# Kernel tuning notes

Hardware: AMD Instinct MI355X
Metric: run time of the kernel (lower is better)

The kernel has to match this reference:

```python
import jax, jax.numpy as jnp
import numpy as np

B, S, H, E = 32, 4096, 512, 512

def setup_inputs() -> dict:
    key = jax.random.key(0)
    ks = jax.random.split(key, 11)
    sc = 1.0 / np.sqrt(H)
    return {
        "context": jax.random.normal(ks[0], (B, S, H), jnp.float32),
        "h": jax.random.normal(ks[1], (B, H), jnp.float32),
        "x": jax.random.normal(ks[2], (B, E), jnp.float32),
        "We": jax.random.normal(ks[3], (H, H), jnp.float32) * sc,
        "be": jax.random.normal(ks[4], (H,), jnp.float32) * sc,
        "Wd": jax.random.normal(ks[5], (H, H), jnp.float32) * sc,
        "bd": jax.random.normal(ks[6], (H,), jnp.float32) * sc,
        "Wv": jax.random.normal(ks[7], (H,), jnp.float32) * sc,
        "bv": jax.random.normal(ks[8], (1,), jnp.float32) * sc,
        "Wr": jax.random.normal(ks[9], (2 * H, 2 * H + E), jnp.float32) * (1.0 / np.sqrt(2 * H + E)),
        "br": jax.random.normal(ks[10], (2 * H,), jnp.float32) * sc,
    }

def reference(context, h, x, We, be, Wd, bd, Wv, bv, Wr, br):
    # gamma_encoder: [B,S,H]; gamma_decoder: [B,1,H]
    ge = jnp.einsum('bsh,kh->bsk', context, We) + be
    gd = h @ Wd.T + bd
    # additive scores -> [B,S]
    scores = jnp.einsum('bsh,h->bs', jnp.tanh(ge + gd[:, None, :]), Wv) + bv[0]
    weights = jax.nn.softmax(scores, axis=1)
    # context vector c_t: [B,H]
    c_t = jnp.einsum('bs,bsh->bh', weights, context)
    # linear_r on [c_t, h, x] -> [B,2H]
    r_t = jnp.concatenate([c_t, h, x], axis=1) @ Wr.T + br
    # maxout over pairs: view [B,H,2].max(-1)
    output = jnp.max(r_t.reshape(-1, r_t.shape[1] // 2, 2), axis=2)
    return (output, weights)
```

## Files before the change

kernel.cpp:

```cpp
#include <hip/hip_runtime.h>

typedef __attribute__((ext_vector_type(8))) short bf16x8;
typedef __attribute__((ext_vector_type(16))) float f32x16;

typedef __attribute__((address_space(3))) unsigned int lds_u32;
typedef __attribute__((address_space(1))) unsigned int glb_u32;

union frag_u { bf16x8 v; unsigned int u[4]; };

__device__ inline unsigned int cvt_pk_bf16(float lo, float hi){
  unsigned int r;
  asm("v_cvt_pk_bf16_f32 %0, %1, %2" : "=v"(r) : "v"(lo), "v"(hi));
  return r;
}
__device__ inline bf16x8 pack8(float4 a, float4 b){
  union { unsigned int u[4]; bf16x8 v; } r;
  r.u[0]=cvt_pk_bf16(a.x,a.y); r.u[1]=cvt_pk_bf16(a.z,a.w);
  r.u[2]=cvt_pk_bf16(b.x,b.y); r.u[3]=cvt_pk_bf16(b.z,b.w);
  return r.v;
}
__device__ inline float fast_tanh(float x){
  float e = __builtin_amdgcn_exp2f(x * 2.8853900817779268f);
  return 1.0f - 2.0f * __builtin_amdgcn_rcpf(e + 1.0f);
}
#define PIN8(F) asm volatile("" : "+v"((F).u[0]), "+v"((F).u[1]), \
                                  "+v"((F).u[2]), "+v"((F).u[3]))
#define LOG2E 1.4426950408889634f

__global__ __launch_bounds__(256) void we_conv(const float* __restrict__ We,
                                               uint4* __restrict__ weFrag){
  int gid = blockIdx.x * 256 + threadIdx.x;
  int l  = gid & 63;
  int nc = gid >> 11;
  int t  = (gid >> 6) & 31;
  int colv = nc*32 + (l & 31);
  int k = t*16 + (l >> 5)*8;
  const float4* src = (const float4*)(We + colv*512 + k);
  float4 f0 = src[0], f1 = src[1];
  weFrag[gid] = make_uint4(cvt_pk_bf16(f0.x,f0.y), cvt_pk_bf16(f0.z,f0.w),
                           cvt_pk_bf16(f1.x,f1.y), cvt_pk_bf16(f1.z,f1.w));
}

__global__ __launch_bounds__(256) void gd_kernel(const float* __restrict__ hvec,
                                                 const float* __restrict__ Wd,
                                                 const float* __restrict__ bd,
                                                 const float* __restrict__ be,
                                                 float* __restrict__ gd){
  __shared__ float hs[512];
  int b = blockIdx.x >> 2, kc = blockIdx.x & 3;
  int tid = threadIdx.x;
  hs[tid]       = hvec[b*512 + tid];
  hs[tid + 256] = hvec[b*512 + 256 + tid];
  __syncthreads();
  int k  = kc*128 + (tid >> 1);
  int hh = (tid & 1) * 256;
  const float4* wrow = (const float4*)(Wd + (size_t)k*512 + hh);
  const float4* hv4  = (const float4*)(hs + hh);
  float acc = 0.f;
  #pragma unroll 8
  for (int i = 0; i < 64; ++i){
    float4 w = wrow[i]; float4 u = hv4[i];
    acc += w.x*u.x + w.y*u.y + w.z*u.z + w.w*u.w;
  }
  acc += __shfl_xor(acc, 1);
  if ((tid & 1) == 0) gd[b*512 + k] = acc + bd[k] + be[k];
}

__global__ __launch_bounds__(256, 2) void score_kernel(
    const float* __restrict__ ctx, const uint4* __restrict__ weFrag,
    const float* __restrict__ gd, const float* __restrict__ Wv,
    float* __restrict__ scores, float* __restrict__ ctp,
    float* __restrict__ MS){
  __shared__ char lds[2*32768 + 4096];
  __shared__ float sc_lds[128];
  __shared__ float w_lds[128];
  __shared__ float red2[2];
  char* ldsB = lds;
  float* gdwv = (float*)(lds + 65536);

  const int tid  = threadIdx.x;
  const int wid  = tid >> 6;
  const int lane = tid & 63;
  const int bid  = blockIdx.x;
  const int row0 = bid * 128;
  const int b    = bid >> 5;
  const int col  = lane & 31;
  const int hi   = lane >> 5;
  const int st   = bid & 15;

  #define ISSUE(NC, BUF) do { \
    const char* _g = (const char*)weFrag + (size_t)(NC)*32768 + wid*8192 + lane*16; \
    char* _l = ldsB + (BUF)*32768 + wid*8192; \
    _Pragma("unroll") \
    for (int _i = 0; _i < 8; ++_i) \
      __builtin_amdgcn_global_load_lds((const glb_u32*)(_g + _i*1024), \
                                       (lds_u32*)(_l + _i*1024), 16, 0, 0); \
  } while(0)

  ISSUE(st, 0);

  if (tid < 128) ((float4*)gdwv)[tid] = ((const float4*)(gd + b*512))[tid];
  else           ((float4*)gdwv)[tid] = ((const float4*)Wv)[tid - 128];

  frag_u afrag[32];
  {
    const float4* ap = (const float4*)(ctx + (size_t)(row0 + wid*32 + col)*512 + hi*8);
    #pragma unroll
    for (int t = 0; t < 32; ++t){
      afrag[t].v = pack8(ap[t*4], ap[t*4 + 1]);
      PIN8(afrag[t]);
    }
  }

  asm volatile("s_waitcnt lgkmcnt(0)" ::: "memory");

  float sc[16];
  #pragma unroll
  for (int r = 0; r < 16; ++r) sc[r] = 0.f;

  for (int nc = 0; nc < 16; ++nc){
    const int cur = (st + nc) & 15;
    asm volatile("s_waitcnt vmcnt(0)" ::: "memory");
    __builtin_amdgcn_s_barrier();
    if (nc < 15) ISSUE((cur + 1) & 15, (nc + 1) & 1);

    const char* bb = ldsB + (nc & 1)*32768 + lane*16;
    f32x16 a0v, a1v, a2v, a3v;
    #pragma unroll
    for (int r = 0; r < 16; ++r){ a0v[r]=0.f; a1v[r]=0.f; a2v[r]=0.f; a3v[r]=0.f; }

    __builtin_amdgcn_s_setprio(1);
    #pragma unroll
    for (int t = 0; t < 8; ++t){
      bf16x8 b0 = *(const bf16x8*)(bb + (t     )*1024);
      bf16x8 b1 = *(const bf16x8*)(bb + (t +  8)*1024);
      bf16x8 b2 = *(const bf16x8*)(bb + (t + 16)*1024);
      bf16x8 b3 = *(const bf16x8*)(bb + (t + 24)*1024);
      a0v = __builtin_amdgcn_mfma_f32_32x32x16_bf16(afrag[t     ].v, b0, a0v, 0, 0, 0);
      a1v = __builtin_amdgcn_mfma_f32_32x32x16_bf16(afrag[t +  8].v, b1, a1v, 0, 0, 0);
      a2v = __builtin_amdgcn_mfma_f32_32x32x16_bf16(afrag[t + 16].v, b2, a2v, 0, 0, 0);
      a3v = __builtin_amdgcn_mfma_f32_32x32x16_bf16(afrag[t + 24].v, b3, a3v, 0, 0, 0);
    }
    __builtin_amdgcn_s_setprio(0);

    float gdv = gdwv[cur*32 + col];
    float wvv = gdwv[512 + cur*32 + col];
    #pragma unroll
    for (int r = 0; r < 16; ++r)
      sc[r] += fast_tanh(((a0v[r] + a1v[r]) + (a2v[r] + a3v[r])) + gdv) * wvv;
  }
  #undef ISSUE

  #pragma unroll
  for (int r = 0; r < 16; ++r){
    #pragma unroll
    for (int m = 1; m <= 16; m <<= 1) sc[r] += __shfl_xor(sc[r], m);
  }
  if (col == 0){
    float* so = scores + row0 + wid*32 + 4*hi;
    #pragma unroll
    for (int r = 0; r < 16; ++r){
      int rr = (r & 3) + 8*(r >> 2);
      so[rr] = sc[r];
      sc_lds[wid*32 + 4*hi + rr] = sc[r];
    }
  }
  __syncthreads();

  float M = -1e30f;
  {
    const float4* s4 = (const float4*)sc_lds;
    #pragma unroll
    for (int i = 0; i < 32; ++i){
      float4 v = s4[i];
      M = fmaxf(M, fmaxf(fmaxf(v.x, v.y), fmaxf(v.z, v.w)));
    }
  }
  if (tid < 128){
    float w = __builtin_amdgcn_exp2f((sc_lds[tid] - M) * LOG2E);
    w_lds[tid] = w;
    #pragma unroll
    for (int o = 1; o < 64; o <<= 1) w += __shfl_xor(w, o);
    if ((tid & 63) == 0) red2[tid >> 6] = w;
  }
  __syncthreads();
  float S_blk = red2[0] + red2[1];

  float ctpA = 0.f, ctpB = 0.f;
  #pragma unroll
  for (int p = 0; p < 2; ++p){
    if ((wid >> 1) == p){
      int rl = (wid & 1)*32 + col;
      char* dst = ldsB + rl*1024;
      int swz = (rl & 7) << 4;
      #pragma unroll
      for (int t = 0; t < 32; ++t)
        *(uint4*)(dst + ((t*32 + hi*16) ^ swz)) = *(uint4*)&afrag[t].u[0];
    }
    __syncthreads();
    const float* wp = w_lds + p*64;
    #pragma unroll 8
    for (int r = 0; r < 64; ++r){
      unsigned int u = *(const unsigned int*)(ldsB + r*1024 + ((tid*4) ^ ((r & 7) << 4)));
      float cw = wp[r];
      union { unsigned int q; float f; } flo, fhi;
      flo.q = u << 16;
      fhi.q = u & 0xffff0000u;
      ctpA += cw * flo.f;
      ctpB += cw * fhi.f;
    }
    __syncthreads();
  }
  ((float2*)(ctp + (size_t)bid*512))[tid] = make_float2(ctpA, ctpB);
  if (tid == 0){ MS[2*bid] = M; MS[2*bid + 1] = S_blk; }
}

__global__ __launch_bounds__(256) void combine_kernel(const float* __restrict__ ctp,
                                                      const float* __restrict__ MS,
                                                      float* __restrict__ ct,
                                                      float* __restrict__ mbuf){
  __shared__ float wsh[32];
  __shared__ float msh[2];
  int b = blockIdx.x, tid = threadIdx.x;
  if (tid < 64){
    int i = tid & 31;
    float Mi = MS[(b*32 + i)*2];
    float Si = MS[(b*32 + i)*2 + 1];
    float M = Mi;
    #pragma unroll
    for (int o = 1; o < 32; o <<= 1) M = fmaxf(M, __shfl_xor(M, o));
    float w = __builtin_amdgcn_exp2f((Mi - M) * LOG2E);
    float d = w * Si;
    #pragma unroll
    for (int o = 1; o < 32; o <<= 1) d += __shfl_xor(d, o);
    if (tid < 32) wsh[i] = w;
    if (tid == 0){ msh[0] = M; msh[1] = 1.0f / d; }
  }
  __syncthreads();
  float invd = msh[1];
  float a0 = 0.f, a1 = 0.f;
  #pragma unroll
  for (int i = 0; i < 32; ++i){
    float2 v = ((const float2*)(ctp + (size_t)(b*32 + i)*512))[tid];
    float w = wsh[i];
    a0 += w * v.x; a1 += w * v.y;
  }
  ((float2*)(ct + b*512))[tid] = make_float2(a0 * invd, a1 * invd);
  if (tid == 0){ mbuf[2*b] = msh[0]; mbuf[2*b + 1] = invd; }
}

__global__ __launch_bounds__(256) void weights_kernel(const float* __restrict__ scores,
                                                      const float* __restrict__ mbuf,
                                                      float* __restrict__ weights){
  int b = blockIdx.x, tid = threadIdx.x;
  float M = mbuf[2*b], invd = mbuf[2*b + 1];
  const float4* src = (const float4*)(scores + b*4096);
  float4* dst = (float4*)(weights + b*4096);
  #pragma unroll
  for (int i = 0; i < 4; ++i){
    float4 v = src[tid + i*256];
    v.x = __builtin_amdgcn_exp2f((v.x - M) * LOG2E) * invd;
    v.y = __builtin_amdgcn_exp2f((v.y - M) * LOG2E) * invd;
    v.z = __builtin_amdgcn_exp2f((v.z - M) * LOG2E) * invd;
    v.w = __builtin_amdgcn_exp2f((v.w - M) * LOG2E) * invd;
    dst[tid + i*256] = v;
  }
}

__global__ __launch_bounds__(256) void final_kernel(
    const float* __restrict__ ct, const float* __restrict__ hvec,
    const float* __restrict__ x, const float* __restrict__ Wr,
    const float* __restrict__ br, float* __restrict__ out){
  __shared__ float xs[8][1536];
  int bt = blockIdx.x >> 4;
  int it = blockIdx.x & 15;
  int tid = threadIdx.x;
  int b0 = bt * 8;
  for (int idx = tid; idx < 8*1536; idx += 256){
    int bl = idx / 1536, j = idx % 1536;
    int b = b0 + bl;
    float v = (j < 512) ? ct[b*512 + j]
            : (j < 1024) ? hvec[b*512 + (j - 512)]
            : x[b*512 + (j - 1024)];
    xs[bl][j] = v;
  }
  __syncthreads();
  int i = it*64 + (tid & 63);
  int bl0 = (tid >> 6) * 2;
  const float4* wrow = (const float4*)(Wr + (size_t)i*1536);
  const float4* x0 = (const float4*)xs[bl0];
  const float4* x1 = (const float4*)xs[bl0 + 1];
  float a0 = 0.f, a1 = 0.f;
  #pragma unroll 4
  for (int k = 0; k < 384; ++k){
    float4 w = wrow[k];
    float4 u0 = x0[k], u1 = x1[k];
    a0 += w.x*u0.x + w.y*u0.y + w.z*u0.z + w.w*u0.w;
    a1 += w.x*u1.x + w.y*u1.y + w.z*u1.z + w.w*u1.w;
  }
  float bias = br[i];
  a0 += bias; a1 += bias;
  float n0 = __shfl_xor(a0, 1);
  float n1 = __shfl_xor(a1, 1);
  if ((tid & 1) == 0){
    out[(b0 + bl0    )*512 + (i >> 1)] = fmaxf(a0, n0);
    out[(b0 + bl0 + 1)*512 + (i >> 1)] = fmaxf(a1, n1);
  }
}

extern "C" void kernel_launch(void* const* d_in, const int* in_sizes, int n_in,
                              void* d_out, int out_size, void* d_ws, size_t ws_size,
                              hipStream_t stream){
  const float* ctx  = (const float*)d_in[0];
  const float* hvec = (const float*)d_in[1];
  const float* x    = (const float*)d_in[2];
  const float* We   = (const float*)d_in[3];
  const float* be   = (const float*)d_in[4];
  const float* Wd   = (const float*)d_in[5];
  const float* bd   = (const float*)d_in[6];
  const float* Wv   = (const float*)d_in[7];
  const float* Wr   = (const float*)d_in[9];
  const float* br   = (const float*)d_in[10];

  float* out     = (float*)d_out;
  float* weights = out + 32*512;

  char* ws = (char*)d_ws;
  char* weFrag   = ws;
  float* scores  = (float*)(ws + (512 << 10));
  float* ctp     = (float*)(ws + (1024 << 10));
  float* MS      = (float*)(ws + (3 << 20));
  float* mbuf    = (float*)(ws + (3 << 20) + (16 << 10));
  float* ct      = (float*)(ws + (3 << 20) + (32 << 10));
  float* gd      = (float*)(ws + (3 << 20) + (96 << 10));

  we_conv<<<128, 256, 0, stream>>>(We, (uint4*)weFrag);
  gd_kernel<<<128, 256, 0, stream>>>(hvec, Wd, bd, be, gd);
  score_kernel<<<1024, 256, 0, stream>>>(ctx, (const uint4*)weFrag, gd, Wv,
                                         scores, ctp, MS);
  combine_kernel<<<32, 256, 0, stream>>>(ctp, MS, ct, mbuf);
  weights_kernel<<<32, 256, 0, stream>>>(scores, mbuf, weights);
  final_kernel<<<64, 256, 0, stream>>>(ct, hvec, x, Wr, br, out);
}
```

Before: 204.2 us.

## Triple-buffer half-chunk We loads and overlap tanh epilogue with next chunk MFMAs

Splits each 32KB We chunk into two 16KB halves held in a three-slot LDS ring, with two halves kept in flight ahead of use. The tanh/score epilogue of the previous chunk is deferred and interleaved between the MFMA groups of the next chunk, so transcendental work can overlap matrix work. LDS drops from about 68KB to about 52KB, which could allow more resident blocks. The context-vector staging now runs in four passes of 32 rows to fit the smaller buffer, which adds barriers.

```diff
diff --git a/kernel.cpp b/kernel.cpp
--- a/kernel.cpp
+++ b/kernel.cpp
@@ -71,12 +71,11 @@
     const float* __restrict__ gd, const float* __restrict__ Wv,
     float* __restrict__ scores, float* __restrict__ ctp,
     float* __restrict__ MS){
-  __shared__ char lds[2*32768 + 4096];
+  __shared__ char ldsB[3*16384];
+  __shared__ float gdwv[1024];
   __shared__ float sc_lds[128];
   __shared__ float w_lds[128];
   __shared__ float red2[2];
-  char* ldsB = lds;
-  float* gdwv = (float*)(lds + 65536);
 
   const int tid  = threadIdx.x;
   const int wid  = tid >> 6;
@@ -88,16 +87,18 @@
   const int hi   = lane >> 5;
   const int st   = bid & 15;
 
-  #define ISSUE(NC, BUF) do { \
-    const char* _g = (const char*)weFrag + (size_t)(NC)*32768 + wid*8192 + lane*16; \
-    char* _l = ldsB + (BUF)*32768 + wid*8192; \
+  #define ISSUE_L(HCL) do { \
+    int _gh = (((st + ((HCL) >> 1)) & 15) << 1) | ((HCL) & 1); \
+    const char* _g = (const char*)weFrag + (size_t)_gh*16384 + wid*4096 + lane*16; \
+    char* _l = ldsB + ((HCL) % 3)*16384 + wid*4096; \
     _Pragma("unroll") \
-    for (int _i = 0; _i < 8; ++_i) \
+    for (int _i = 0; _i < 4; ++_i) \
       __builtin_amdgcn_global_load_lds((const glb_u32*)(_g + _i*1024), \
                                        (lds_u32*)(_l + _i*1024), 16, 0, 0); \
   } while(0)
 
-  ISSUE(st, 0);
+  ISSUE_L(0);
+  ISSUE_L(1);
 
   if (tid < 128) ((float4*)gdwv)[tid] = ((const float4*)(gd + b*512))[tid];
   else           ((float4*)gdwv)[tid] = ((const float4*)Wv)[tid - 128];
@@ -114,42 +115,76 @@
 
   asm volatile("s_waitcnt lgkmcnt(0)" ::: "memory");
 
-  float sc[16];
+  float sc[16], pend[16];
+  float pGd = 0.f, pWv = 0.f;
   #pragma unroll
   for (int r = 0; r < 16; ++r) sc[r] = 0.f;
+
+  f32x16 a0v, a1v, a2v, a3v;
+
+  #define MGROUP(BB, H, TG) do { \
+    const char* _bb = (BB); \
+    bf16x8 b0 = *(const bf16x8*)(_bb + ((TG)*4 + 0)*1024); \
+    bf16x8 b1 = *(const bf16x8*)(_bb + ((TG)*4 + 1)*1024); \
+    bf16x8 b2 = *(const bf16x8*)(_bb + ((TG)*4 + 2)*1024); \
+    bf16x8 b3 = *(const bf16x8*)(_bb + ((TG)*4 + 3)*1024); \
+    a0v = __builtin_amdgcn_mfma_f32_32x32x16_bf16(afrag[(H)*16 + (TG)*4 + 0].v, b0, a0v, 0, 0, 0); \
+    a1v = __builtin_amdgcn_mfma_f32_32x32x16_bf16(afrag[(H)*16 + (TG)*4 + 1].v, b1, a1v, 0, 0, 0); \
+    a2v = __builtin_amdgcn_mfma_f32_32x32x16_bf16(afrag[(H)*16 + (TG)*4 + 2].v, b2, a2v, 0, 0, 0); \
+    a3v = __builtin_amdgcn_mfma_f32_32x32x16_bf16(afrag[(H)*16 + (TG)*4 + 3].v, b3, a3v, 0, 0, 0); \
+  } while(0)
+
+  #define TANH4(TG) do { \
+    sc[(TG)*4 + 0] += fast_tanh(pend[(TG)*4 + 0] + pGd) * pWv; \
+    sc[(TG)*4 + 1] += fast_tanh(pend[(TG)*4 + 1] + pGd) * pWv; \
+    sc[(TG)*4 + 2] += fast_tanh(pend[(TG)*4 + 2] + pGd) * pWv; \
+    sc[(TG)*4 + 3] += fast_tanh(pend[(TG)*4 + 3] + pGd) * pWv; \
+  } while(0)
 
   for (int nc = 0; nc < 16; ++nc){
     const int cur = (st + nc) & 15;
-    asm volatile("s_waitcnt vmcnt(0)" ::: "memory");
+    const int hc  = 2*nc;
+
+    #pragma unroll
+    for (int r = 0; r < 16; ++r){ a0v[r]=0.f; a1v[r]=0.f; a2v[r]=0.f; a3v[r]=0.f; }
+
+    asm volatile("s_waitcnt vmcnt(4)" ::: "memory");
     __builtin_amdgcn_s_barrier();
-    if (nc < 15) ISSUE((cur + 1) & 15, (nc + 1) & 1);
-
-    const char* bb = ldsB + (nc & 1)*32768 + lane*16;
-    f32x16 a0v, a1v, a2v, a3v;
-    #pragma unroll
-    for (int r = 0; r < 16; ++r){ a0v[r]=0.f; a1v[r]=0.f; a2v[r]=0.f; a3v[r]=0.f; }
-
-    __builtin_amdgcn_s_setprio(1);
-    #pragma unroll
-    for (int t = 0; t < 8; ++t){
-      bf16x8 b0 = *(const bf16x8*)(bb + (t     )*1024);
-      bf16x8 b1 = *(const bf16x8*)(bb + (t +  8)*1024);
-      bf16x8 b2 = *(const bf16x8*)(bb + (t + 16)*1024);
-      bf16x8 b3 = *(const bf16x8*)(bb + (t + 24)*1024);
-      a0v = __builtin_amdgcn_mfma_f32_32x32x16_bf16(afrag[t     ].v, b0, a0v, 0, 0, 0);
-      a1v = __builtin_amdgcn_mfma_f32_32x32x16_bf16(afrag[t +  8].v, b1, a1v, 0, 0, 0);
-      a2v = __builtin_amdgcn_mfma_f32_32x32x16_bf16(afrag[t + 16].v, b2, a2v, 0, 0, 0);
-      a3v = __builtin_amdgcn_mfma_f32_32x32x16_bf16(afrag[t + 24].v, b3, a3v, 0, 0, 0);
-    }
-    __builtin_amdgcn_s_setprio(0);
-
-    float gdv = gdwv[cur*32 + col];
-    float wvv = gdwv[512 + cur*32 + col];
+    if (nc < 15) ISSUE_L(hc + 2);
+    {
+      const char* bb = ldsB + (hc % 3)*16384 + lane*16;
+      __builtin_amdgcn_s_setprio(1);
+      MGROUP(bb, 0, 0); if (nc > 0) TANH4(0);
+      MGROUP(bb, 0, 1); if (nc > 0) TANH4(1);
+      MGROUP(bb, 0, 2); if (nc > 0) TANH4(2);
+      MGROUP(bb, 0, 3); if (nc > 0) TANH4(3);
+      __builtin_amdgcn_s_setprio(0);
+    }
+
+    if (nc < 15) asm volatile("s_waitcnt vmcnt(4)" ::: "memory");
+    else         asm volatile("s_waitcnt vmcnt(0)" ::: "memory");
+    __builtin_amdgcn_s_barrier();
+    if (nc < 15) ISSUE_L(hc + 3);
+    {
+      const char* bb = ldsB + ((hc + 1) % 3)*16384 + lane*16;
+      __builtin_amdgcn_s_setprio(1);
+      MGROUP(bb, 1, 0);
+      MGROUP(bb, 1, 1);
+      MGROUP(bb, 1, 2);
+      MGROUP(bb, 1, 3);
+      __builtin_amdgcn_s_setprio(0);
+    }
+
     #pragma unroll
     for (int r = 0; r < 16; ++r)
-      sc[r] += fast_tanh(((a0v[r] + a1v[r]) + (a2v[r] + a3v[r])) + gdv) * wvv;
-  }
-  #undef ISSUE
+      pend[r] = (a0v[r] + a1v[r]) + (a2v[r] + a3v[r]);
+    pGd = gdwv[cur*32 + col];
+    pWv = gdwv[512 + cur*32 + col];
+  }
+  TANH4(0); TANH4(1); TANH4(2); TANH4(3);
+  #undef ISSUE_L
+  #undef MGROUP
+  #undef TANH4
 
   #pragma unroll
   for (int r = 0; r < 16; ++r){
@@ -188,9 +223,9 @@
 
   float ctpA = 0.f, ctpB = 0.f;
   #pragma unroll
-  for (int p = 0; p < 2; ++p){
-    if ((wid >> 1) == p){
-      int rl = (wid & 1)*32 + col;
+  for (int p = 0; p < 4; ++p){
+    if (wid == p){
+      int rl = col;
       char* dst = ldsB + rl*1024;
       int swz = (rl & 7) << 4;
       #pragma unroll
@@ -198,9 +233,9 @@
         *(uint4*)(dst + ((t*32 + hi*16) ^ swz)) = *(uint4*)&afrag[t].u[0];
     }
     __syncthreads();
-    const float* wp = w_lds + p*64;
+    const float* wp = w_lds + p*32;
     #pragma unroll 8
-    for (int r = 0; r < 64; ++r){
+    for (int r = 0; r < 32; ++r){
       unsigned int u = *(const unsigned int*)(ldsB + r*1024 + ((tid*4) ^ ((r & 7) << 4)));
       float cw = wp[r];
       union { unsigned int q; float f; } flo, fhi;
```

After: 206.1 us. No clear change (+0.9%).

## Double score block to 512 threads sharing each We chunk across 256 rows

Applied to the files above, without the earlier changes.

The score kernel now runs 512-thread blocks covering 256 context rows each, so every We chunk staged in LDS is shared by eight waves instead of four. Each wave issues half as many global-to-LDS loads, which halves total We traffic into LDS. Launch bounds change to (512,1), the MFMA priority hints are removed, and the context-partial pass gives each thread one column. The combine kernel is reworked for 16 partials per batch. The trade-off is a larger block with more barrier participants and possibly different occupancy, given the large per-thread A-fragment register footprint.

```diff
diff --git a/kernel.cpp b/kernel.cpp
--- a/kernel.cpp
+++ b/kernel.cpp
@@ -66,41 +66,40 @@
   if ((tid & 1) == 0) gd[b*512 + k] = acc + bd[k] + be[k];
 }
 
-__global__ __launch_bounds__(256, 2) void score_kernel(
+__global__ __launch_bounds__(512, 1) void score_kernel(
     const float* __restrict__ ctx, const uint4* __restrict__ weFrag,
     const float* __restrict__ gd, const float* __restrict__ Wv,
     float* __restrict__ scores, float* __restrict__ ctp,
     float* __restrict__ MS){
-  __shared__ char lds[2*32768 + 4096];
-  __shared__ float sc_lds[128];
-  __shared__ float w_lds[128];
-  __shared__ float red2[2];
-  char* ldsB = lds;
-  float* gdwv = (float*)(lds + 65536);
+  __shared__ char ldsB[2*32768];
+  __shared__ float gdwv[1024];
+  __shared__ float sc_lds[256];
+  __shared__ float w_lds[256];
+  __shared__ float red4[4];
 
   const int tid  = threadIdx.x;
   const int wid  = tid >> 6;
   const int lane = tid & 63;
   const int bid  = blockIdx.x;
-  const int row0 = bid * 128;
-  const int b    = bid >> 5;
+  const int row0 = bid * 256;
+  const int b    = bid >> 4;
   const int col  = lane & 31;
   const int hi   = lane >> 5;
   const int st   = bid & 15;
 
   #define ISSUE(NC, BUF) do { \
-    const char* _g = (const char*)weFrag + (size_t)(NC)*32768 + wid*8192 + lane*16; \
-    char* _l = ldsB + (BUF)*32768 + wid*8192; \
+    const char* _g = (const char*)weFrag + (size_t)(NC)*32768 + wid*4096 + lane*16; \
+    char* _l = ldsB + (BUF)*32768 + wid*4096; \
     _Pragma("unroll") \
-    for (int _i = 0; _i < 8; ++_i) \
+    for (int _i = 0; _i < 4; ++_i) \
       __builtin_amdgcn_global_load_lds((const glb_u32*)(_g + _i*1024), \
                                        (lds_u32*)(_l + _i*1024), 16, 0, 0); \
   } while(0)
 
   ISSUE(st, 0);
 
-  if (tid < 128) ((float4*)gdwv)[tid] = ((const float4*)(gd + b*512))[tid];
-  else           ((float4*)gdwv)[tid] = ((const float4*)Wv)[tid - 128];
+  if (tid < 128)      ((float4*)gdwv)[tid] = ((const float4*)(gd + b*512))[tid];
+  else if (tid < 256) ((float4*)gdwv)[tid] = ((const float4*)Wv)[tid - 128];
 
   frag_u afrag[32];
   {
@@ -129,7 +128,6 @@
     #pragma unroll
     for (int r = 0; r < 16; ++r){ a0v[r]=0.f; a1v[r]=0.f; a2v[r]=0.f; a3v[r]=0.f; }
 
-    __builtin_amdgcn_s_setprio(1);
     #pragma unroll
     for (int t = 0; t < 8; ++t){
       bf16x8 b0 = *(const bf16x8*)(bb + (t     )*1024);
@@ -141,7 +139,6 @@
       a2v = __builtin_amdgcn_mfma_f32_32x32x16_bf16(afrag[t + 16].v, b2, a2v, 0, 0, 0);
       a3v = __builtin_amdgcn_mfma_f32_32x32x16_bf16(afrag[t + 24].v, b3, a3v, 0, 0, 0);
     }
-    __builtin_amdgcn_s_setprio(0);
 
     float gdv = gdwv[cur*32 + col];
     float wvv = gdwv[512 + cur*32 + col];
@@ -171,24 +168,24 @@
   {
     const float4* s4 = (const float4*)sc_lds;
     #pragma unroll
-    for (int i = 0; i < 32; ++i){
+    for (int i = 0; i < 64; ++i){
       float4 v = s4[i];
       M = fmaxf(M, fmaxf(fmaxf(v.x, v.y), fmaxf(v.z, v.w)));
     }
   }
-  if (tid < 128){
+  if (tid < 256){
     float w = __builtin_amdgcn_exp2f((sc_lds[tid] - M) * LOG2E);
     w_lds[tid] = w;
     #pragma unroll
     for (int o = 1; o < 64; o <<= 1) w += __shfl_xor(w, o);
-    if ((tid & 63) == 0) red2[tid >> 6] = w;
-  }
-  __syncthreads();
-  float S_blk = red2[0] + red2[1];
-
-  float ctpA = 0.f, ctpB = 0.f;
-  #pragma unroll
-  for (int p = 0; p < 2; ++p){
+    if ((tid & 63) == 0) red4[tid >> 6] = w;
+  }
+  __syncthreads();
+  float S_blk = red4[0] + red4[1] + red4[2] + red4[3];
+
+  float ctp1 = 0.f;
+  #pragma unroll
+  for (int p = 0; p < 4; ++p){
     if ((wid >> 1) == p){
       int rl = (wid & 1)*32 + col;
       char* dst = ldsB + rl*1024;
@@ -201,17 +198,13 @@
     const float* wp = w_lds + p*64;
     #pragma unroll 8
     for (int r = 0; r < 64; ++r){
-      unsigned int u = *(const unsigned int*)(ldsB + r*1024 + ((tid*4) ^ ((r & 7) << 4)));
-      float cw = wp[r];
-      union { unsigned int q; float f; } flo, fhi;
-      flo.q = u << 16;
-      fhi.q = u & 0xffff0000u;
-      ctpA += cw * flo.f;
-      ctpB += cw * fhi.f;
+      unsigned int u = *(const unsigned short*)(ldsB + r*1024 + ((tid*2) ^ ((r & 7) << 4)));
+      union { unsigned int q; float f; } fv; fv.q = u << 16;
+      ctp1 += wp[r] * fv.f;
     }
     __syncthreads();
   }
-  ((float2*)(ctp + (size_t)bid*512))[tid] = make_float2(ctpA, ctpB);
+  ctp[(size_t)bid*512 + tid] = ctp1;
   if (tid == 0){ MS[2*bid] = M; MS[2*bid + 1] = S_blk; }
 }
 
@@ -219,29 +212,28 @@
                                                       const float* __restrict__ MS,
                                                       float* __restrict__ ct,
                                                       float* __restrict__ mbuf){
-  __shared__ float wsh[32];
+  __shared__ float wsh[16];
   __shared__ float msh[2];
   int b = blockIdx.x, tid = threadIdx.x;
-  if (tid < 64){
-    int i = tid & 31;
-    float Mi = MS[(b*32 + i)*2];
-    float Si = MS[(b*32 + i)*2 + 1];
+  if (tid < 16){
+    float Mi = MS[(b*16 + tid)*2];
+    float Si = MS[(b*16 + tid)*2 + 1];
     float M = Mi;
     #pragma unroll
-    for (int o = 1; o < 32; o <<= 1) M = fmaxf(M, __shfl_xor(M, o));
+    for (int o = 1; o < 16; o <<= 1) M = fmaxf(M, __shfl_xor(M, o));
     float w = __builtin_amdgcn_exp2f((Mi - M) * LOG2E);
     float d = w * Si;
     #pragma unroll
-    for (int o = 1; o < 32; o <<= 1) d += __shfl_xor(d, o);
-    if (tid < 32) wsh[i] = w;
+    for (int o = 1; o < 16; o <<= 1) d += __shfl_xor(d, o);
+    wsh[tid] = w;
     if (tid == 0){ msh[0] = M; msh[1] = 1.0f / d; }
   }
   __syncthreads();
   float invd = msh[1];
   float a0 = 0.f, a1 = 0.f;
   #pragma unroll
-  for (int i = 0; i < 32; ++i){
-    float2 v = ((const float2*)(ctp + (size_t)(b*32 + i)*512))[tid];
+  for (int i = 0; i < 16; ++i){
+    float2 v = ((const float2*)(ctp + (size_t)(b*16 + i)*512))[tid];
     float w = wsh[i];
     a0 += w * v.x; a1 += w * v.y;
   }
@@ -336,8 +328,8 @@
 
   we_conv<<<128, 256, 0, stream>>>(We, (uint4*)weFrag);
   gd_kernel<<<128, 256, 0, stream>>>(hvec, Wd, bd, be, gd);
-  score_kernel<<<1024, 256, 0, stream>>>(ctx, (const uint4*)weFrag, gd, Wv,
-                                         scores, ctp, MS);
+  score_kernel<<<512, 512, 0, stream>>>(ctx, (const uint4*)weFrag, gd, Wv,
+                                        scores, ctp, MS);
   combine_kernel<<<32, 256, 0, stream>>>(ctp, MS, ct, mbuf);
   weights_kernel<<<32, 256, 0, stream>>>(scores, mbuf, weights);
   final_kernel<<<64, 256, 0, stream>>>(ct, hvec, x, Wr, br, out);
```

Result: no change. 206.6 us (+1.2%).

## Triple-buffer half-chunk We loads and store context partials as bf16

Applied to the files above, without the earlier changes.

The We fragment layout is reordered into 16 KB half-chunks, and the score loop uses a three-stage LDS ring with partial vmcnt waits, so the next loads stay in flight while the MFMAs run. One accumulator is used instead of four, and the per-block start-offset rotation is dropped. The context-vector partials are written as packed bf16, which halves the partial traffic into the combine kernel and adds extra rounding. LDS use drops, which may help occupancy, but there are twice as many barriers and the MFMA dependency chain is serialized.

```diff
diff --git a/kernel.cpp b/kernel.cpp
--- a/kernel.cpp
+++ b/kernel.cpp
@@ -5,8 +5,6 @@
 
 typedef __attribute__((address_space(3))) unsigned int lds_u32;
 typedef __attribute__((address_space(1))) unsigned int glb_u32;
-
-union frag_u { bf16x8 v; unsigned int u[4]; };
 
 __device__ inline unsigned int cvt_pk_bf16(float lo, float hi){
   unsigned int r;
@@ -23,18 +21,15 @@
   float e = __builtin_amdgcn_exp2f(x * 2.8853900817779268f);
   return 1.0f - 2.0f * __builtin_amdgcn_rcpf(e + 1.0f);
 }
-#define PIN8(F) asm volatile("" : "+v"((F).u[0]), "+v"((F).u[1]), \
-                                  "+v"((F).u[2]), "+v"((F).u[3]))
 #define LOG2E 1.4426950408889634f
 
 __global__ __launch_bounds__(256) void we_conv(const float* __restrict__ We,
                                                uint4* __restrict__ weFrag){
   int gid = blockIdx.x * 256 + threadIdx.x;
   int l  = gid & 63;
-  int nc = gid >> 11;
-  int t  = (gid >> 6) & 31;
-  int colv = nc*32 + (l & 31);
-  int k = t*16 + (l >> 5)*8;
+  int hc = gid >> 10;
+  int colv = (hc >> 1)*32 + (l & 31);
+  int k = ((hc & 1) << 8) + ((gid >> 6) & 15)*16 + (l >> 5)*8;
   const float4* src = (const float4*)(We + colv*512 + k);
   float4 f0 = src[0], f1 = src[1];
   weFrag[gid] = make_uint4(cvt_pk_bf16(f0.x,f0.y), cvt_pk_bf16(f0.z,f0.w),
@@ -67,16 +62,15 @@
 }
 
 __global__ __launch_bounds__(256, 2) void score_kernel(
-    const float* __restrict__ ctx, const uint4* __restrict__ weFrag,
+    const float* __restrict__ ctx, const char* __restrict__ weFrag,
     const float* __restrict__ gd, const float* __restrict__ Wv,
-    float* __restrict__ scores, float* __restrict__ ctp,
+    float* __restrict__ scores, unsigned int* __restrict__ ctp,
     float* __restrict__ MS){
-  __shared__ char lds[2*32768 + 4096];
+  __shared__ char lds[3*16384 + 4096];
   __shared__ float sc_lds[128];
   __shared__ float w_lds[128];
   __shared__ float red2[2];
-  char* ldsB = lds;
-  float* gdwv = (float*)(lds + 65536);
+  float* gdwv = (float*)(lds + 49152);
 
   const int tid  = threadIdx.x;
   const int wid  = tid >> 6;
@@ -86,68 +80,78 @@
   const int b    = bid >> 5;
   const int col  = lane & 31;
   const int hi   = lane >> 5;
-  const int st   = bid & 15;
-
-  #define ISSUE(NC, BUF) do { \
-    const char* _g = (const char*)weFrag + (size_t)(NC)*32768 + wid*8192 + lane*16; \
-    char* _l = ldsB + (BUF)*32768 + wid*8192; \
+
+  if (tid < 128) ((float4*)gdwv)[tid] = ((const float4*)(gd + b*512))[tid];
+  else           ((float4*)gdwv)[tid] = ((const float4*)Wv)[tid - 128];
+
+  bf16x8 afrag[32];
+  {
+    const float4* ap = (const float4*)(ctx + (size_t)(row0 + wid*32 + col)*512 + hi*8);
+    #pragma unroll
+    for (int t = 0; t < 32; ++t)
+      afrag[t] = pack8(ap[t*4], ap[t*4 + 1]);
+  }
+
+  asm volatile("s_waitcnt lgkmcnt(0)" ::: "memory");
+
+  #define ISSUE(HC, BUF) do { \
+    const char* _g = weFrag + ((size_t)(HC))*16384 + wid*4096; \
+    char* _l = lds + (BUF)*16384 + wid*4096; \
     _Pragma("unroll") \
-    for (int _i = 0; _i < 8; ++_i) \
-      __builtin_amdgcn_global_load_lds((const glb_u32*)(_g + _i*1024), \
+    for (int _i = 0; _i < 4; ++_i) \
+      __builtin_amdgcn_global_load_lds((const glb_u32*)(_g + _i*1024 + lane*16), \
                                        (lds_u32*)(_l + _i*1024), 16, 0, 0); \
   } while(0)
 
-  ISSUE(st, 0);
-
-  if (tid < 128) ((float4*)gdwv)[tid] = ((const float4*)(gd + b*512))[tid];
-  else           ((float4*)gdwv)[tid] = ((const float4*)Wv)[tid - 128];
-
-  frag_u afrag[32];
-  {
-    const float4* ap = (const float4*)(ctx + (size_t)(row0 + wid*32 + col)*512 + hi*8);
-    #pragma unroll
-    for (int t = 0; t < 32; ++t){
-      afrag[t].v = pack8(ap[t*4], ap[t*4 + 1]);
-      PIN8(afrag[t]);
-    }
-  }
-
-  asm volatile("s_waitcnt lgkmcnt(0)" ::: "memory");
-
+  ISSUE(0, 0);
+  ISSUE(1, 1);
+
+  f32x16 acc;
   float sc[16];
   #pragma unroll
   for (int r = 0; r < 16; ++r) sc[r] = 0.f;
 
   for (int nc = 0; nc < 16; ++nc){
-    const int cur = (st + nc) & 15;
-    asm volatile("s_waitcnt vmcnt(0)" ::: "memory");
+    const int hc0 = 2*nc, hc1 = 2*nc + 1;
+
+    asm volatile("s_waitcnt vmcnt(4)" ::: "memory");
     __builtin_amdgcn_s_barrier();
-    if (nc < 15) ISSUE((cur + 1) & 15, (nc + 1) & 1);
-
-    const char* bb = ldsB + (nc & 1)*32768 + lane*16;
-    f32x16 a0v, a1v, a2v, a3v;
-    #pragma unroll
-    for (int r = 0; r < 16; ++r){ a0v[r]=0.f; a1v[r]=0.f; a2v[r]=0.f; a3v[r]=0.f; }
-
-    __builtin_amdgcn_s_setprio(1);
-    #pragma unroll
-    for (int t = 0; t < 8; ++t){
-      bf16x8 b0 = *(const bf16x8*)(bb + (t     )*1024);
-      bf16x8 b1 = *(const bf16x8*)(bb + (t +  8)*1024);
-      bf16x8 b2 = *(const bf16x8*)(bb + (t + 16)*1024);
-      bf16x8 b3 = *(const bf16x8*)(bb + (t + 24)*1024);
-      a0v = __builtin_amdgcn_mfma_f32_32x32x16_bf16(afrag[t     ].v, b0, a0v, 0, 0, 0);
-      a1v = __builtin_amdgcn_mfma_f32_32x32x16_bf16(afrag[t +  8].v, b1, a1v, 0, 0, 0);
-      a2v = __builtin_amdgcn_mfma_f32_32x32x16_bf16(afrag[t + 16].v, b2, a2v, 0, 0, 0);
-      a3v = __builtin_amdgcn_mfma_f32_32x32x16_bf16(afrag[t + 24].v, b3, a3v, 0, 0, 0);
-    }
-    __builtin_amdgcn_s_setprio(0);
-
-    float gdv = gdwv[cur*32 + col];
-    float wvv = gdwv[512 + cur*32 + col];
-    #pragma unroll
-    for (int r = 0; r < 16; ++r)
-      sc[r] += fast_tanh(((a0v[r] + a1v[r]) + (a2v[r] + a3v[r])) + gdv) * wvv;
+    if (hc0 < 30) ISSUE(hc0 + 2, (hc0 + 2) % 3);
+    {
+      const char* bb = lds + (hc0 % 3)*16384 + lane*16;
+      #pragma unroll
+      for (int r = 0; r < 16; ++r) acc[r] = 0.f;
+      __builtin_amdgcn_s_setprio(1);
+      #pragma unroll
+      for (int t = 0; t < 16; ++t){
+        bf16x8 bf = *(const bf16x8*)(bb + t*1024);
+        acc = __builtin_amdgcn_mfma_f32_32x32x16_bf16(afrag[t], bf, acc, 0, 0, 0);
+      }
+      __builtin_amdgcn_s_setprio(0);
+    }
+
+    if (nc < 15) asm volatile("s_waitcnt vmcnt(4)" ::: "memory");
+    else         asm volatile("s_waitcnt vmcnt(0)" ::: "memory");
+    __builtin_amdgcn_s_barrier();
+    if (hc1 < 30) ISSUE(hc1 + 2, (hc1 + 2) % 3);
+    {
+      const char* bb = lds + (hc1 % 3)*16384 + lane*16;
+      __builtin_amdgcn_s_setprio(1);
+      #pragma unroll
+      for (int t = 0; t < 16; ++t){
+        bf16x8 bf = *(const bf16x8*)(bb + t*1024);
+        acc = __builtin_amdgcn_mfma_f32_32x32x16_bf16(afrag[16 + t], bf, acc, 0, 0, 0);
+      }
+      __builtin_amdgcn_s_setprio(0);
+    }
+
+    {
+      float gdv = gdwv[nc*32 + col];
+      float wvv = gdwv[512 + nc*32 + col];
+      #pragma unroll
+      for (int r = 0; r < 16; ++r)
+        sc[r] += fast_tanh(acc[r] + gdv) * wvv;
+    }
   }
   #undef ISSUE
 
@@ -157,12 +161,13 @@
     for (int m = 1; m <= 16; m <<= 1) sc[r] += __shfl_xor(sc[r], m);
   }
   if (col == 0){
-    float* so = scores + row0 + wid*32 + 4*hi;
+    int rbase = wid*32 + 4*hi;
+    float* so = scores + row0 + rbase;
     #pragma unroll
     for (int r = 0; r < 16; ++r){
       int rr = (r & 3) + 8*(r >> 2);
       so[rr] = sc[r];
-      sc_lds[wid*32 + 4*hi + rr] = sc[r];
+      sc_lds[rbase + rr] = sc[r];
     }
   }
   __syncthreads();
@@ -186,46 +191,47 @@
   __syncthreads();
   float S_blk = red2[0] + red2[1];
 
-  float ctpA = 0.f, ctpB = 0.f;
+  float cA = 0.f, cB = 0.f;
   #pragma unroll
-  for (int p = 0; p < 2; ++p){
-    if ((wid >> 1) == p){
-      int rl = (wid & 1)*32 + col;
-      char* dst = ldsB + rl*1024;
+  for (int p = 0; p < 4; ++p){
+    if (wid == p){
+      int rl = col;
+      char* dst = lds + rl*1024;
       int swz = (rl & 7) << 4;
       #pragma unroll
-      for (int t = 0; t < 32; ++t)
-        *(uint4*)(dst + ((t*32 + hi*16) ^ swz)) = *(uint4*)&afrag[t].u[0];
+      for (int t = 0; t < 32; ++t){
+        union { bf16x8 v; uint4 q; } u; u.v = afrag[t];
+        *(uint4*)(dst + ((t*32 + hi*16) ^ swz)) = u.q;
+      }
     }
     __syncthreads();
-    const float* wp = w_lds + p*64;
+    const float* wp = w_lds + p*32;
     #pragma unroll 8
-    for (int r = 0; r < 64; ++r){
-      unsigned int u = *(const unsigned int*)(ldsB + r*1024 + ((tid*4) ^ ((r & 7) << 4)));
+    for (int r = 0; r < 32; ++r){
+      unsigned int u = *(const unsigned int*)(lds + r*1024 + ((tid*4) ^ ((r & 7) << 4)));
       float cw = wp[r];
       union { unsigned int q; float f; } flo, fhi;
       flo.q = u << 16;
       fhi.q = u & 0xffff0000u;
-      ctpA += cw * flo.f;
-      ctpB += cw * fhi.f;
+      cA += cw * flo.f;
+      cB += cw * fhi.f;
     }
     __syncthreads();
   }
-  ((float2*)(ctp + (size_t)bid*512))[tid] = make_float2(ctpA, ctpB);
+  ctp[(size_t)bid*256 + tid] = cvt_pk_bf16(cA, cB);
   if (tid == 0){ MS[2*bid] = M; MS[2*bid + 1] = S_blk; }
 }
 
-__global__ __launch_bounds__(256) void combine_kernel(const float* __restrict__ ctp,
+__global__ __launch_bounds__(256) void combine_kernel(const unsigned int* __restrict__ ctp,
                                                       const float* __restrict__ MS,
                                                       float* __restrict__ ct,
                                                       float* __restrict__ mbuf){
   __shared__ float wsh[32];
   __shared__ float msh[2];
   int b = blockIdx.x, tid = threadIdx.x;
-  if (tid < 64){
-    int i = tid & 31;
-    float Mi = MS[(b*32 + i)*2];
-    float Si = MS[(b*32 + i)*2 + 1];
+  if (tid < 32){
+    float Mi = MS[(b*32 + tid)*2];
+    float Si = MS[(b*32 + tid)*2 + 1];
     float M = Mi;
     #pragma unroll
     for (int o = 1; o < 32; o <<= 1) M = fmaxf(M, __shfl_xor(M, o));
@@ -233,17 +239,21 @@
     float d = w * Si;
     #pragma unroll
     for (int o = 1; o < 32; o <<= 1) d += __shfl_xor(d, o);
-    if (tid < 32) wsh[i] = w;
+    wsh[tid] = w;
     if (tid == 0){ msh[0] = M; msh[1] = 1.0f / d; }
   }
   __syncthreads();
   float invd = msh[1];
   float a0 = 0.f, a1 = 0.f;
-  #pragma unroll
+  #pragma unroll 8
   for (int i = 0; i < 32; ++i){
-    float2 v = ((const float2*)(ctp + (size_t)(b*32 + i)*512))[tid];
+    unsigned int u = ctp[(size_t)(b*32 + i)*256 + tid];
     float w = wsh[i];
-    a0 += w * v.x; a1 += w * v.y;
+    union { unsigned int q; float f; } flo, fhi;
+    flo.q = u << 16;
+    fhi.q = u & 0xffff0000u;
+    a0 += w * flo.f;
+    a1 += w * fhi.f;
   }
   ((float2*)(ct + b*512))[tid] = make_float2(a0 * invd, a1 * invd);
   if (tid == 0){ mbuf[2*b] = msh[0]; mbuf[2*b + 1] = invd; }
@@ -328,16 +338,15 @@
   char* ws = (char*)d_ws;
   char* weFrag   = ws;
   float* scores  = (float*)(ws + (512 << 10));
-  float* ctp     = (float*)(ws + (1024 << 10));
-  float* MS      = (float*)(ws + (3 << 20));
-  float* mbuf    = (float*)(ws + (3 << 20) + (16 << 10));
-  float* ct      = (float*)(ws + (3 << 20) + (32 << 10));
-  float* gd      = (float*)(ws + (3 << 20) + (96 << 10));
+  unsigned int* ctp = (unsigned int*)(ws + (1024 << 10));
+  float* MS      = (float*)(ws + (2 << 20));
+  float* mbuf    = (float*)(ws + (2 << 20) + (16 << 10));
+  float* ct      = (float*)(ws + (2 << 20) + (32 << 10));
+  float* gd      = (float*)(ws + (2 << 20) + (96 << 10));
 
   we_conv<<<128, 256, 0, stream>>>(We, (uint4*)weFrag);
   gd_kernel<<<128, 256, 0, stream>>>(hvec, Wd, bd, be, gd);
-  score_kernel<<<1024, 256, 0, stream>>>(ctx, (const uint4*)weFrag, gd, Wv,
-                                         scores, ctp, MS);
+  score_kernel<<<1024, 256, 0, stream>>>(ctx, weFrag, gd, Wv, scores, ctp, MS);
   combine_kernel<<<32, 256, 0, stream>>>(ctp, MS, ct, mbuf);
   weights_kernel<<<32, 256, 0, stream>>>(scores, mbuf, weights);
   final_kernel<<<64, 256, 0, stream>>>(ct, hvec, x, Wr, br, out);
```

New measurement: 196.6 us. -3.7%, faster.
